# Optimization experiments

Hardware: AMD Instinct MI355X
Metric: run time of the kernel (lower is better)

The kernel has to match this reference:

```python
import jax, jax.numpy as jnp
import numpy as np

D = 1024
H = 16
DH = D // H


def setup_inputs() -> dict:
    key = jax.random.key(0)
    ks = jax.random.split(key, 12)
    s = 0.02
    return {
        "x": jax.random.normal(ks[0], (2, 2048, D), dtype=jnp.float32),
        "ln1_g": jnp.ones((D,), jnp.float32),
        "ln1_b": jnp.zeros((D,), jnp.float32),
        "W_attn": jax.random.normal(ks[1], (3 * D, D), jnp.float32) * s,
        "b_attn": jnp.zeros((3 * D,), jnp.float32),
        "W_proj": jax.random.normal(ks[2], (D, D), jnp.float32) * s,
        "b_proj": jnp.zeros((D,), jnp.float32),
        "ln2_g": jnp.ones((D,), jnp.float32),
        "ln2_b": jnp.zeros((D,), jnp.float32),
        "W_up": jax.random.normal(ks[3], (4 * D, D), jnp.float32) * s,
        "b_up": jnp.zeros((4 * D,), jnp.float32),
        "W_down": jax.random.normal(ks[4], (D, 4 * D), jnp.float32) * s,
        "b_down": jnp.zeros((D,), jnp.float32),
    }


def layernorm(x, g, b, eps=1e-5):
    mu = jnp.mean(x, axis=-1, keepdims=True)
    var = jnp.mean(jnp.square(x - mu), axis=-1, keepdims=True)
    return (x - mu) * jax.lax.rsqrt(var + eps) * g + b


def new_gelu(x):
    c = np.sqrt(2.0 / np.pi).astype(np.float32)
    return 0.5 * x * (1.0 + jnp.tanh(c * (x + 0.044715 * x ** 3)))


def reference(x, ln1_g, ln1_b, W_attn, b_attn, W_proj, b_proj, ln2_g, ln2_b, W_up, b_up, W_down, b_down):
    b, s, d = x.shape
    h = layernorm(x, ln1_g, ln1_b)
    qkv = h @ W_attn.T + b_attn  # [b,s,3d]
    q, k, v = jnp.split(qkv, 3, axis=-1)
    # [b, H, s, DH]
    q = q.reshape(b, s, H, DH).transpose(0, 2, 1, 3)
    k = k.reshape(b, s, H, DH).transpose(0, 2, 1, 3)
    v = v.reshape(b, s, H, DH).transpose(0, 2, 1, 3)
    scores = jnp.einsum("bhqd,bhkd->bhqk", q, k) / np.sqrt(DH).astype(np.float32)
    causal = jnp.tril(jnp.ones((s, s), dtype=bool))
    scores = jnp.where(causal, scores, -jnp.inf)
    attn = jax.nn.softmax(scores, axis=-1)
    o = jnp.einsum("bhqk,bhkd->bhqd", attn, v).transpose(0, 2, 1, 3).reshape(b, s, d)
    x = x + o @ W_proj.T + b_proj
    h2 = layernorm(x, ln2_g, ln2_b)
    mlp = new_gelu(h2 @ W_up.T + b_up) @ W_down.T + b_down
    return x + mlp
```

## Files before the change

### kernel.cpp

```cpp
#include <hip/hip_runtime.h>
#include <hip/hip_bf16.h>

typedef __hip_bfloat16 bf16;
using bf16x8 = __attribute__((ext_vector_type(8))) short;
using bf16x4 = __attribute__((ext_vector_type(4))) short;
using f32x4  = __attribute__((ext_vector_type(4))) float;

#define D_MODEL 1024
#define SEQ     2048
#define NTOK    4096
#define NHEAD   16
#define DHEAD   64

__device__ inline f32x4 mfma16(bf16x8 a, bf16x8 b, f32x4 c) {
  return __builtin_amdgcn_mfma_f32_16x16x32_bf16(a, b, c, 0, 0, 0);
}

__device__ inline f32x4 mfma16k16(bf16x4 a, bf16x4 b, f32x4 c) {
#if __has_builtin(__builtin_amdgcn_mfma_f32_16x16x16bf16_1k)
  return __builtin_amdgcn_mfma_f32_16x16x16bf16_1k(a, b, c, 0, 0, 0);
#else
  f32x4 d;
  asm("v_mfma_f32_16x16x16_bf16 %0, %1, %2, %3" : "=v"(d) : "v"(a), "v"(b), "v"(c));
  return d;
#endif
}

__device__ inline void glds16(const void* g, void* l) {
  __builtin_amdgcn_global_load_lds(
      (const __attribute__((address_space(1))) unsigned int*)g,
      (__attribute__((address_space(3))) unsigned int*)l, 16, 0, 0);
}

__global__ __launch_bounds__(256) void f2bf4_kernel(const float* __restrict__ s0,
                                                    const float* __restrict__ s1,
                                                    const float* __restrict__ s2,
                                                    const float* __restrict__ s3,
                                                    bf16* __restrict__ dst) {
  const size_t M1 = (size_t)D_MODEL * D_MODEL;
  size_t i = ((size_t)blockIdx.x * 256 + threadIdx.x) * 4;
  const float* s; size_t off;
  if (i < 3 * M1)      { s = s0; off = i; }
  else if (i < 4 * M1) { s = s1; off = i - 3 * M1; }
  else if (i < 8 * M1) { s = s2; off = i - 4 * M1; }
  else                 { s = s3; off = i - 8 * M1; }
  float4 v = *(const float4*)(s + off);
  dst[i + 0] = __float2bfloat16(v.x);
  dst[i + 1] = __float2bfloat16(v.y);
  dst[i + 2] = __float2bfloat16(v.z);
  dst[i + 3] = __float2bfloat16(v.w);
}

__global__ __launch_bounds__(256) void ln_kernel(const float* __restrict__ x,
                                                 const float* __restrict__ g,
                                                 const float* __restrict__ bta,
                                                 bf16* __restrict__ out) {
  int row = blockIdx.x;
  int tid = threadIdx.x;
  const float* xr = x + (size_t)row * D_MODEL;
  float4 v = *(const float4*)(xr + tid * 4);
  float s  = v.x + v.y + v.z + v.w;
  float s2 = v.x * v.x + v.y * v.y + v.z * v.z + v.w * v.w;
  for (int o = 32; o > 0; o >>= 1) {
    s  += __shfl_down(s, o);
    s2 += __shfl_down(s2, o);
  }
  __shared__ float red[8];
  int wave = tid >> 6, lane = tid & 63;
  if (lane == 0) { red[wave] = s; red[4 + wave] = s2; }
  __syncthreads();
  s  = red[0] + red[1] + red[2] + red[3];
  s2 = red[4] + red[5] + red[6] + red[7];
  float mu  = s * (1.f / D_MODEL);
  float var = s2 * (1.f / D_MODEL) - mu * mu;
  float rs  = rsqrtf(var + 1e-5f);
  float4 gv = *(const float4*)(g + tid * 4);
  float4 bv = *(const float4*)(bta + tid * 4);
  bf16* orow = out + (size_t)row * D_MODEL + tid * 4;
  orow[0] = __float2bfloat16((v.x - mu) * rs * gv.x + bv.x);
  orow[1] = __float2bfloat16((v.y - mu) * rs * gv.y + bv.y);
  orow[2] = __float2bfloat16((v.z - mu) * rs * gv.z + bv.z);
  orow[3] = __float2bfloat16((v.w - mu) * rs * gv.w + bv.w);
}

#define EP_BIAS_BF16      0
#define EP_BIAS_GELU_BF16 1
#define EP_BIAS_RES_F32   2

template <int EP>
__device__ inline void ep_store(void* out, const float* res, size_t off, float v) {
  if (EP == EP_BIAS_BF16) {
    ((bf16*)out)[off] = __float2bfloat16(v);
  } else if (EP == EP_BIAS_GELU_BF16) {
    float u = 0.7978845608f * (v + 0.044715f * v * v * v);
    float gl = v / (1.0f + __expf(-2.0f * u));
    ((bf16*)out)[off] = __float2bfloat16(gl);
  } else {
    ((float*)out)[off] = res[off] + v;
  }
}

template <int EP>
__global__ __launch_bounds__(256, 3) void gemm_nt(const bf16* __restrict__ A,
                                                  const bf16* __restrict__ W,
                                                  const float* __restrict__ bias,
                                                  const float* res, void* out,
                                                  int M, int N, int K) {
  __shared__ short sA[128 * 64];
  __shared__ short sB[128 * 64];
  int tid  = threadIdx.x;
  int wave = tid >> 6, lane = tid & 63;
  int quad = lane >> 4, l16 = lane & 15;
  int wm = (wave >> 1) * 64, wn = (wave & 1) * 64;
  int bm = blockIdx.x * 128, bn = blockIdx.y * 128;

  int rl = lane >> 3;
  int cz = (lane & 7) ^ rl;
  const bf16* aptr[4];
  const bf16* bptr[4];
#pragma unroll
  for (int i = 0; i < 4; i++) {
    int j = wave * 4 + i;
    aptr[i] = A + (size_t)(bm + j * 8 + rl) * K + cz * 8;
    bptr[i] = W + (size_t)(bn + j * 8 + rl) * K + cz * 8;
  }

  f32x4 acc[4][4] = {};

  for (int k0 = 0; k0 < K; k0 += 64) {
    __syncthreads();
#pragma unroll
    for (int i = 0; i < 4; i++) {
      glds16(aptr[i] + k0, (char*)sA + (wave * 4 + i) * 1024);
      glds16(bptr[i] + k0, (char*)sB + (wave * 4 + i) * 1024);
    }
    __builtin_amdgcn_s_waitcnt(0);
    __syncthreads();

#pragma unroll
    for (int kk = 0; kk < 2; kk++) {
      int cq = kk * 4 + quad;
      int sw = (cq ^ (l16 & 7)) * 8;
      bf16x8 af[4], bfr[4];
#pragma unroll
      for (int t = 0; t < 4; t++) {
        af[t]  = *(const bf16x8*)&sA[(wm + t * 16 + l16) * 64 + sw];
        bfr[t] = *(const bf16x8*)&sB[(wn + t * 16 + l16) * 64 + sw];
      }
#pragma unroll
      for (int mt = 0; mt < 4; mt++)
#pragma unroll
        for (int nt = 0; nt < 4; nt++)
          acc[mt][nt] = mfma16(af[mt], bfr[nt], acc[mt][nt]);
    }
  }

#pragma unroll
  for (int mt = 0; mt < 4; mt++)
#pragma unroll
    for (int nt = 0; nt < 4; nt++) {
      int col = bn + wn + nt * 16 + l16;
      float bs = bias[col];
#pragma unroll
      for (int i = 0; i < 4; i++) {
        int row = bm + wm + mt * 16 + quad * 4 + i;
        ep_store<EP>(out, res, (size_t)row * N + col, acc[mt][nt][i] + bs);
      }
    }
}

template <int EP>
__global__ __launch_bounds__(256, 3) void gemm_nt2(const bf16* __restrict__ A,
                                                   const bf16* __restrict__ W,
                                                   const float* __restrict__ bias,
                                                   const float* res, void* out,
                                                   int M, int N, int K) {
  __shared__ short sA[128 * 64];
  __shared__ short sB[64 * 64];
  int tid  = threadIdx.x;
  int wave = tid >> 6, lane = tid & 63;
  int quad = lane >> 4, l16 = lane & 15;
  int wm = wave * 32;
  int bm = blockIdx.x * 128, bn = blockIdx.y * 64;

  int rl = lane >> 3;
  int cz = (lane & 7) ^ rl;
  const bf16* aptr[4];
  const bf16* bptr[2];
#pragma unroll
  for (int i = 0; i < 4; i++)
    aptr[i] = A + (size_t)(bm + (wave * 4 + i) * 8 + rl) * K + cz * 8;
#pragma unroll
  for (int i = 0; i < 2; i++)
    bptr[i] = W + (size_t)(bn + (wave * 2 + i) * 8 + rl) * K + cz * 8;

  f32x4 acc[2][4] = {};

  for (int k0 = 0; k0 < K; k0 += 64) {
    __syncthreads();
#pragma unroll
    for (int i = 0; i < 4; i++)
      glds16(aptr[i] + k0, (char*)sA + (wave * 4 + i) * 1024);
#pragma unroll
    for (int i = 0; i < 2; i++)
      glds16(bptr[i] + k0, (char*)sB + (wave * 2 + i) * 1024);
    __builtin_amdgcn_s_waitcnt(0);
    __syncthreads();

#pragma unroll
    for (int kk = 0; kk < 2; kk++) {
      int cq = kk * 4 + quad;
      int sw = (cq ^ (l16 & 7)) * 8;
      bf16x8 af[2], bfr[4];
#pragma unroll
      for (int t = 0; t < 2; t++)
        af[t] = *(const bf16x8*)&sA[(wm + t * 16 + l16) * 64 + sw];
#pragma unroll
      for (int t = 0; t < 4; t++)
        bfr[t] = *(const bf16x8*)&sB[(t * 16 + l16) * 64 + sw];
#pragma unroll
      for (int mt = 0; mt < 2; mt++)
#pragma unroll
        for (int nt = 0; nt < 4; nt++)
          acc[mt][nt] = mfma16(af[mt], bfr[nt], acc[mt][nt]);
    }
  }

#pragma unroll
  for (int mt = 0; mt < 2; mt++)
#pragma unroll
    for (int nt = 0; nt < 4; nt++) {
      int col = bn + nt * 16 + l16;
      float bs = bias[col];
#pragma unroll
      for (int i = 0; i < 4; i++) {
        int row = bm + wm + mt * 16 + quad * 4 + i;
        ep_store<EP>(out, res, (size_t)row * N + col, acc[mt][nt][i] + bs);
      }
    }
}

__global__ __launch_bounds__(256, 2) void attn_kernel(const short* __restrict__ qkvS,
                                                      short* __restrict__ oS) {
  int bh = blockIdx.y;
  int b = bh >> 4, h = bh & 15;
  int iq = blockIdx.x;
  int qa = iq * 64, qb = (31 - iq) * 64;
  int tid = threadIdx.x, wave = tid >> 6, lane = tid & 63;
  int quad = lane >> 4, l16 = lane & 15;
  const int RS = 3 * D_MODEL;
  const short* base = qkvS + (size_t)b * SEQ * RS;
  const int koff = D_MODEL + h * 64, voff = 2 * D_MODEL + h * 64, qoff = h * 64;
  const float c2 = 0.1803368801f;

  __shared__ short sK[64 * 64];
  __shared__ short sV[64 * 64];

  int rl = lane >> 3, cz = (lane & 7) ^ rl;
  int vkr = tid >> 3, vd0 = (tid & 7) * 8;
  int vb7 = tid & 7;
  int kv3 = vkr & 3;
  int c4lo = vkr >> 2, c4hi = c4lo + 8;
  int xpar = (c4lo & 1) << 3;

  int qrA = qa + wave * 16 + l16, qrB = qb + wave * 16 + l16;
  bf16x8 qA0 = *(const bf16x8*)&base[(size_t)qrA * RS + qoff + quad * 8];
  bf16x8 qA1 = *(const bf16x8*)&base[(size_t)qrA * RS + qoff + 32 + quad * 8];
  bf16x8 qB0 = *(const bf16x8*)&base[(size_t)qrB * RS + qoff + quad * 8];
  bf16x8 qB1 = *(const bf16x8*)&base[(size_t)qrB * RS + qoff + 32 + quad * 8];

  f32x4 oA[4] = {}, oB[4] = {};
  float lsA = 0.f, lsB = 0.f;
  int ntile = 32 - iq;

  bf16x8 v0, v1;
  {
    const short* vp = &base[(size_t)vkr * RS + voff + vd0];
    v0 = *(const bf16x8*)vp;
    v1 = *(const bf16x8*)(vp + (size_t)32 * RS);
  }

  for (int t = 0; t < ntile; t++) {
    int kv0 = t * 64;
    __syncthreads();
#pragma unroll
    for (int ii = 0; ii < 2; ii++) {
      int j = wave * 2 + ii;
      glds16(&base[(size_t)(kv0 + j * 8 + rl) * RS + koff + cz * 8], (char*)sK + j * 1024);
    }
    __asm__ __volatile__("" ::: "memory");

    bf16x8 nv0, nv1;
    bool more = (t + 1 < ntile);
    if (more) {
      const short* vp = &base[(size_t)((t + 1) * 64 + vkr) * RS + voff + vd0];
      nv0 = *(const bf16x8*)vp;
      nv1 = *(const bf16x8*)(vp + (size_t)32 * RS);
    }

#pragma unroll
    for (int j = 0; j < 8; j++)
      sV[c4lo * 256 + (vb7 | ((j << 3) ^ xpar)) * 4 + kv3] = v0[j];
#pragma unroll
    for (int j = 0; j < 8; j++)
      sV[c4hi * 256 + (vb7 | ((j << 3) ^ xpar)) * 4 + kv3] = v1[j];

    __asm__ __volatile__("" ::: "memory");
    if (more) __builtin_amdgcn_s_waitcnt(0x0002);
    else      __builtin_amdgcn_s_waitcnt(0x0000);
    __builtin_amdgcn_s_barrier();
    __asm__ __volatile__("" ::: "memory");

    auto do_q = [&](bf16x8 q0, bf16x8 q1, f32x4* oo, float& ls, bool diag, int qg) {
      f32x4 st[4];
#pragma unroll
      for (int t16 = 0; t16 < 4; t16++) {
        bf16x8 kf0 = *(const bf16x8*)&sK[(t16 * 16 + l16) * 64 + ((quad ^ (l16 & 7)) * 8)];
        bf16x8 kf1 = *(const bf16x8*)&sK[(t16 * 16 + l16) * 64 + (((quad + 4) ^ (l16 & 7)) * 8)];
        f32x4 z = {};
        z = mfma16(kf0, q0, z);
        st[t16] = mfma16(kf1, q1, z);
      }
#pragma unroll
      for (int t16 = 0; t16 < 4; t16++) {
        bf16x4 pf;
        int kvb = kv0 + t16 * 16 + quad * 4;
#pragma unroll
        for (int e = 0; e < 4; e++) {
          float p = exp2f(fminf(st[t16][e] * c2, 30.f));
          if (diag && (kvb + e > qg)) p = 0.f;
          ls += p;
          pf[e] = __builtin_bit_cast(short, __float2bfloat16(p));
        }
        int c4r = t16 * 4 + quad;
        int xr = (c4r & 1) << 3;
#pragma unroll
        for (int dt = 0; dt < 4; dt++) {
          int pr = (dt * 16 + l16) ^ xr;
          bf16x4 vb = *(const bf16x4*)&sV[c4r * 256 + pr * 4];
          oo[dt] = mfma16k16(pf, vb, oo[dt]);
        }
      }
    };

    do_q(qB0, qB1, oB, lsB, t == ntile - 1, qb + wave * 16 + l16);
    if (t <= iq) do_q(qA0, qA1, oA, lsA, t == iq, qa + wave * 16 + l16);

    if (more) { v0 = nv0; v1 = nv1; }
  }

  auto finish = [&](f32x4* oo, float ls, int q0p) {
    ls += __shfl_xor(ls, 16);
    ls += __shfl_xor(ls, 32);
    float inv[4];
#pragma unroll
    for (int e = 0; e < 4; e++) inv[e] = 1.0f / __shfl(ls, quad * 4 + e);
    int sigbase = ((l16 & 7) << 3) | (l16 >> 3);
#pragma unroll
    for (int dt = 0; dt < 4; dt++)
#pragma unroll
      for (int e = 0; e < 4; e++) {
        int row = q0p + wave * 16 + quad * 4 + e;
        oS[((size_t)b * SEQ + row) * D_MODEL + qoff + sigbase + dt * 2] =
            __builtin_bit_cast(short, __float2bfloat16(oo[dt][e] * inv[e]));
      }
  };
  finish(oB, lsB, qb);
  finish(oA, lsA, qa);
}

extern "C" void kernel_launch(void* const* d_in, const int* in_sizes, int n_in,
                              void* d_out, int out_size, void* d_ws, size_t ws_size,
                              hipStream_t stream) {
  const float* x      = (const float*)d_in[0];
  const float* ln1_g  = (const float*)d_in[1];
  const float* ln1_b  = (const float*)d_in[2];
  const float* W_attn = (const float*)d_in[3];
  const float* b_attn = (const float*)d_in[4];
  const float* W_proj = (const float*)d_in[5];
  const float* b_proj = (const float*)d_in[6];
  const float* ln2_g  = (const float*)d_in[7];
  const float* ln2_b  = (const float*)d_in[8];
  const float* W_up   = (const float*)d_in[9];
  const float* b_up   = (const float*)d_in[10];
  const float* W_down = (const float*)d_in[11];
  const float* b_down = (const float*)d_in[12];
  float* out = (float*)d_out;

  char* p = (char*)d_ws;
  bf16* Wattn_b = (bf16*)p; p += (size_t)3 * D_MODEL * D_MODEL * 2;
  bf16* Wproj_b = (bf16*)p; p += (size_t)D_MODEL * D_MODEL * 2;
  bf16* Wup_b   = (bf16*)p; p += (size_t)4 * D_MODEL * D_MODEL * 2;
  bf16* Wdown_b = (bf16*)p; p += (size_t)4 * D_MODEL * D_MODEL * 2;
  bf16* h_b     = (bf16*)p; p += (size_t)NTOK * D_MODEL * 2;
  bf16* qkv_b   = (bf16*)p; p += (size_t)NTOK * 3 * D_MODEL * 2;
  bf16* o_b     = (bf16*)p; p += (size_t)NTOK * D_MODEL * 2;
  bf16* h2_b    = (bf16*)p; p += (size_t)NTOK * D_MODEL * 2;
  bf16* up_b    = (bf16*)p; p += (size_t)NTOK * 4 * D_MODEL * 2;

  {
    size_t ntot = (size_t)12 * D_MODEL * D_MODEL;
    f2bf4_kernel<<<(int)(ntot / 1024), 256, 0, stream>>>(W_attn, W_proj, W_up, W_down, Wattn_b);
  }
  ln_kernel<<<NTOK, 256, 0, stream>>>(x, ln1_g, ln1_b, h_b);
  gemm_nt<EP_BIAS_BF16><<<dim3(NTOK / 128, 3 * D_MODEL / 128), 256, 0, stream>>>(
      h_b, Wattn_b, b_attn, nullptr, qkv_b, NTOK, 3 * D_MODEL, D_MODEL);
  attn_kernel<<<dim3(16, 2 * NHEAD), 256, 0, stream>>>((const short*)qkv_b, (short*)o_b);
  gemm_nt2<EP_BIAS_RES_F32><<<dim3(NTOK / 128, D_MODEL / 64), 256, 0, stream>>>(
      o_b, Wproj_b, b_proj, x, out, NTOK, D_MODEL, D_MODEL);
  ln_kernel<<<NTOK, 256, 0, stream>>>(out, ln2_g, ln2_b, h2_b);
  gemm_nt<EP_BIAS_GELU_BF16><<<dim3(NTOK / 128, 4 * D_MODEL / 128), 256, 0, stream>>>(
      h2_b, Wup_b, b_up, nullptr, up_b, NTOK, 4 * D_MODEL, D_MODEL);
  gemm_nt2<EP_BIAS_RES_F32><<<dim3(NTOK / 128, D_MODEL / 64), 256, 0, stream>>>(
      up_b, Wdown_b, b_down, out, out, NTOK, D_MODEL, 4 * D_MODEL);
}
```

Measured before the change: 341.8 us.

## Register-prefetch K tiles and share K fragment loads across both query blocks

Replaces the async global-to-LDS copy of K tiles with register prefetching of the next K tile, mirroring the existing V prefetch, then storing both into LDS after a barrier. The QK^T stage now loads each K fragment from LDS once and issues MFMAs for both query blocks A and B, instead of reloading K per block. Barriers are rewritten as explicit lgkmcnt waits plus s_barrier. This raises register pressure and may reduce occupancy, and it drops the direct-to-LDS load path.

```diff
diff --git a/kernel.cpp b/kernel.cpp
--- a/kernel.cpp
+++ b/kernel.cpp
@@ -273,80 +273,88 @@
   float lsA = 0.f, lsB = 0.f;
   int ntile = 32 - iq;
 
-  bf16x8 v0, v1;
+  bf16x8 kc0, kc1, vc0, vc1;
   {
+    const short* kp = &base[(size_t)(wave * 16 + rl) * RS + koff + cz * 8];
+    kc0 = *(const bf16x8*)kp;
+    kc1 = *(const bf16x8*)(kp + (size_t)8 * RS);
     const short* vp = &base[(size_t)vkr * RS + voff + vd0];
-    v0 = *(const bf16x8*)vp;
-    v1 = *(const bf16x8*)(vp + (size_t)32 * RS);
-  }
+    vc0 = *(const bf16x8*)vp;
+    vc1 = *(const bf16x8*)(vp + (size_t)32 * RS);
+  }
+
+  auto ptail = [&](const f32x4* st, f32x4* oo, float& ls, bool diag, int qg, int kv0) {
+#pragma unroll
+    for (int t16 = 0; t16 < 4; t16++) {
+      bf16x4 pf;
+      int kvb = kv0 + t16 * 16 + quad * 4;
+#pragma unroll
+      for (int e = 0; e < 4; e++) {
+        float p = exp2f(fminf(st[t16][e] * c2, 30.f));
+        if (diag && (kvb + e > qg)) p = 0.f;
+        ls += p;
+        pf[e] = __builtin_bit_cast(short, __float2bfloat16(p));
+      }
+      int c4r = t16 * 4 + quad;
+      int xr = (c4r & 1) << 3;
+#pragma unroll
+      for (int dt = 0; dt < 4; dt++) {
+        int pr = (dt * 16 + l16) ^ xr;
+        bf16x4 vb = *(const bf16x4*)&sV[c4r * 256 + pr * 4];
+        oo[dt] = mfma16k16(pf, vb, oo[dt]);
+      }
+    }
+  };
 
   for (int t = 0; t < ntile; t++) {
     int kv0 = t * 64;
-    __syncthreads();
-#pragma unroll
-    for (int ii = 0; ii < 2; ii++) {
-      int j = wave * 2 + ii;
-      glds16(&base[(size_t)(kv0 + j * 8 + rl) * RS + koff + cz * 8], (char*)sK + j * 1024);
-    }
-    __asm__ __volatile__("" ::: "memory");
-
-    bf16x8 nv0, nv1;
+    asm volatile("s_waitcnt lgkmcnt(0)" ::: "memory");
+    asm volatile("s_barrier" ::: "memory");
+
+    bf16x8 kn0, kn1, vn0, vn1;
     bool more = (t + 1 < ntile);
     if (more) {
-      const short* vp = &base[(size_t)((t + 1) * 64 + vkr) * RS + voff + vd0];
-      nv0 = *(const bf16x8*)vp;
-      nv1 = *(const bf16x8*)(vp + (size_t)32 * RS);
-    }
-
+      int kvn = kv0 + 64;
+      const short* kp = &base[(size_t)(kvn + wave * 16 + rl) * RS + koff + cz * 8];
+      kn0 = *(const bf16x8*)kp;
+      kn1 = *(const bf16x8*)(kp + (size_t)8 * RS);
+      const short* vp = &base[(size_t)(kvn + vkr) * RS + voff + vd0];
+      vn0 = *(const bf16x8*)vp;
+      vn1 = *(const bf16x8*)(vp + (size_t)32 * RS);
+    }
+
+    *(bf16x8*)&sK[(wave * 2 + 0) * 512 + lane * 8] = kc0;
+    *(bf16x8*)&sK[(wave * 2 + 1) * 512 + lane * 8] = kc1;
 #pragma unroll
     for (int j = 0; j < 8; j++)
-      sV[c4lo * 256 + (vb7 | ((j << 3) ^ xpar)) * 4 + kv3] = v0[j];
+      sV[c4lo * 256 + (vb7 | ((j << 3) ^ xpar)) * 4 + kv3] = vc0[j];
 #pragma unroll
     for (int j = 0; j < 8; j++)
-      sV[c4hi * 256 + (vb7 | ((j << 3) ^ xpar)) * 4 + kv3] = v1[j];
-
-    __asm__ __volatile__("" ::: "memory");
-    if (more) __builtin_amdgcn_s_waitcnt(0x0002);
-    else      __builtin_amdgcn_s_waitcnt(0x0000);
-    __builtin_amdgcn_s_barrier();
-    __asm__ __volatile__("" ::: "memory");
-
-    auto do_q = [&](bf16x8 q0, bf16x8 q1, f32x4* oo, float& ls, bool diag, int qg) {
-      f32x4 st[4];
-#pragma unroll
-      for (int t16 = 0; t16 < 4; t16++) {
-        bf16x8 kf0 = *(const bf16x8*)&sK[(t16 * 16 + l16) * 64 + ((quad ^ (l16 & 7)) * 8)];
-        bf16x8 kf1 = *(const bf16x8*)&sK[(t16 * 16 + l16) * 64 + (((quad + 4) ^ (l16 & 7)) * 8)];
-        f32x4 z = {};
-        z = mfma16(kf0, q0, z);
-        st[t16] = mfma16(kf1, q1, z);
-      }
-#pragma unroll
-      for (int t16 = 0; t16 < 4; t16++) {
-        bf16x4 pf;
-        int kvb = kv0 + t16 * 16 + quad * 4;
-#pragma unroll
-        for (int e = 0; e < 4; e++) {
-          float p = exp2f(fminf(st[t16][e] * c2, 30.f));
-          if (diag && (kvb + e > qg)) p = 0.f;
-          ls += p;
-          pf[e] = __builtin_bit_cast(short, __float2bfloat16(p));
-        }
-        int c4r = t16 * 4 + quad;
-        int xr = (c4r & 1) << 3;
-#pragma unroll
-        for (int dt = 0; dt < 4; dt++) {
-          int pr = (dt * 16 + l16) ^ xr;
-          bf16x4 vb = *(const bf16x4*)&sV[c4r * 256 + pr * 4];
-          oo[dt] = mfma16k16(pf, vb, oo[dt]);
-        }
-      }
-    };
-
-    do_q(qB0, qB1, oB, lsB, t == ntile - 1, qb + wave * 16 + l16);
-    if (t <= iq) do_q(qA0, qA1, oA, lsA, t == iq, qa + wave * 16 + l16);
-
-    if (more) { v0 = nv0; v1 = nv1; }
+      sV[c4hi * 256 + (vb7 | ((j << 3) ^ xpar)) * 4 + kv3] = vc1[j];
+
+    asm volatile("s_waitcnt lgkmcnt(0)" ::: "memory");
+    asm volatile("s_barrier" ::: "memory");
+
+    bool doA = (t <= iq);
+    int xk = l16 & 7;
+    f32x4 stB[4], stA[4];
+#pragma unroll
+    for (int t16 = 0; t16 < 4; t16++) {
+      bf16x8 kf0 = *(const bf16x8*)&sK[(t16 * 16 + l16) * 64 + ((quad ^ xk) * 8)];
+      bf16x8 kf1 = *(const bf16x8*)&sK[(t16 * 16 + l16) * 64 + (((quad + 4) ^ xk) * 8)];
+      f32x4 z = {};
+      z = mfma16(kf0, qB0, z);
+      stB[t16] = mfma16(kf1, qB1, z);
+      if (doA) {
+        f32x4 za = {};
+        za = mfma16(kf0, qA0, za);
+        stA[t16] = mfma16(kf1, qA1, za);
+      }
+    }
+    ptail(stB, oB, lsB, t == ntile - 1, qb + wave * 16 + l16, kv0);
+    if (doA) ptail(stA, oA, lsA, t == iq, qa + wave * 16 + l16, kv0);
+
+    if (more) { kc0 = kn0; kc1 = kn1; vc0 = vn0; vc1 = vn1; }
   }
 
   auto finish = [&](f32x4* oo, float ls, int q0p) {
```

Result: slower. 356.3 us (+4.2%).
